# Kernel tuning notes

Hardware: AMD Instinct MI355X
Metric: run time of the kernel (lower is better)

The kernel has to match this reference:

```python
import jax, jax.numpy as jnp
import numpy as np

N, E, IN_C, HID, OUT_C = 50000, 800000, 128, 64, 64
NEG_SLOPE = 0.2
BN_EPS = 1e-5


def _gat(x, edges, W, a_src, a_dst, b):
    """PyG-style GATConv: linear -> per-head attention logits -> softmax over
    incoming edges (self-loops added, as in PyG default) -> weighted scatter-add."""
    n = x.shape[0]
    H, C = a_src.shape
    xw = (x @ W).reshape(n, H, C)                      # [N,H,C]
    loop = jnp.arange(n)
    src = jnp.concatenate([edges[0], loop])            # [E+N]
    dst = jnp.concatenate([edges[1], loop])
    al_s = jnp.sum(xw * a_src, axis=-1)                # [N,H]
    al_d = jnp.sum(xw * a_dst, axis=-1)
    e = jax.nn.leaky_relu(al_s[src] + al_d[dst], NEG_SLOPE)   # [E+N,H]
    emax = jax.ops.segment_max(e, dst, num_segments=n)        # stable softmax per target
    w = jnp.exp(e - emax[dst])
    denom = jax.ops.segment_sum(w, dst, num_segments=n)
    alpha = w / (denom[dst] + 1e-16)                   # [E+N,H]
    msg = xw[src] * alpha[:, :, None]                  # [E+N,H,C]
    out = jax.ops.segment_sum(msg, dst, num_segments=n)       # [N,H,C]
    return out.reshape(n, H * C) + b


def _bn(x, g, be):
    # BatchNorm1d training-mode forward: biased batch statistics over nodes.
    m = jnp.mean(x, axis=0)
    v = jnp.mean((x - m) ** 2, axis=0)
    return (x - m) * jax.lax.rsqrt(v + BN_EPS) * g + be


def setup_inputs() -> dict:
    key = jax.random.key(0)
    ks = jax.random.split(key, 20)
    p = lambda k, s: (jax.random.normal(k, s, jnp.float32) * 0.1)
    return {
        "x": jax.random.normal(ks[0], (1, N, IN_C), jnp.float32),
        "adj": jax.random.randint(ks[1], (2, E), 0, N),
        # conv1: in=128 -> hidden=64, heads=2 (concat -> 128)
        "W1": p(ks[2], (IN_C, 2 * HID)), "as1": p(ks[3], (2, HID)), "ad1": p(ks[4], (2, HID)), "b1": jnp.zeros((2 * HID,), jnp.float32),
        "g1": jnp.ones((2 * HID,), jnp.float32), "be1": jnp.zeros((2 * HID,), jnp.float32),
        # conv2: 128 -> 64, heads=2
        "W2": p(ks[5], (2 * HID, 2 * HID)), "as2": p(ks[6], (2, HID)), "ad2": p(ks[7], (2, HID)), "b2": jnp.zeros((2 * HID,), jnp.float32),
        "g2": jnp.ones((2 * HID,), jnp.float32), "be2": jnp.zeros((2 * HID,), jnp.float32),
        # conv3: 128 -> 64, heads=1
        "W3": p(ks[8], (2 * HID, OUT_C)), "as3": p(ks[9], (1, OUT_C)), "ad3": p(ks[10], (1, OUT_C)), "b3": jnp.zeros((OUT_C,), jnp.float32),
        "g3": jnp.ones((OUT_C,), jnp.float32), "be3": jnp.zeros((OUT_C,), jnp.float32),
    }


def reference(x, adj, W1, as1, ad1, b1, g1, be1, W2, as2, ad2, b2, g2, be2, W3, as3, ad3, b3, g3, be3):
    x0 = x[0]                                          # squeeze batch dim
    x1 = _bn(jax.nn.relu(_gat(x0, adj, W1, as1, ad1, b1)), g1, be1)   # [N,128]
    x2 = _bn(jax.nn.relu(_gat(x1, adj, W2, as2, ad2, b2)), g2, be2)   # [N,128]
    x3 = _bn(jax.nn.relu(_gat(x2, adj, W3, as3, ad3, b3)), g3, be3)   # [N,64]
    return jnp.concatenate([x1, x2, x3], axis=-1)      # [N,320]
```

## Files before the change

### kernel.cpp

```cpp
#include <hip/hip_runtime.h>

typedef unsigned int uint;
typedef unsigned short ushort;


static __device__ __forceinline__ ushort bf16_rne(float x) {
    uint u = __float_as_uint(x);
    return (ushort)((u + 0x7fffu + ((u >> 16) & 1u)) >> 16);
}
static __device__ __forceinline__ float bf16_f(ushort h) {
    return __uint_as_float(((uint)h) << 16);
}

__global__ __launch_bounds__(256) void k_bcount(const int* __restrict__ dst, int e,
                                                int* __restrict__ bcntp) {
    __shared__ int h[512];
    int tid = threadIdx.x;
    h[tid] = 0;
    h[tid + 256] = 0;
    __syncthreads();
    int stride = gridDim.x * 256;
    for (int i = blockIdx.x * 256 + tid; i < e; i += stride)
        atomicAdd(&h[dst[i] >> 7], 1);
    __syncthreads();
    if (h[tid]) atomicAdd(&bcntp[tid * 16], h[tid]);
    if (h[tid + 256]) atomicAdd(&bcntp[(tid + 256) * 16], h[tid + 256]);
}

__global__ __launch_bounds__(512) void k_bscan(const int* __restrict__ bcntp,
                                               int* __restrict__ bbase,
                                               int* __restrict__ bcurp, int nb, int n,
                                               int total, int* __restrict__ row_start) {
    __shared__ int s[512];
    int tid = threadIdx.x;
    int v = 0;
    if (tid < nb) v = bcntp[tid * 16] + min(128, n - (tid << 7));
    s[tid] = v;
    __syncthreads();
    for (int off = 1; off < 512; off <<= 1) {
        int t = (tid >= off) ? s[tid - off] : 0;
        __syncthreads();
        s[tid] += t;
        __syncthreads();
    }
    if (tid < nb) {
        int excl = s[tid] - v;
        bbase[tid] = excl;
        bcurp[tid * 16] = excl;
    }
    if (tid == 0) {
        bbase[nb] = total;
        row_start[n] = total;
    }
}

__global__ __launch_bounds__(512) void k_bscatter(const int* __restrict__ src,
                                                  const int* __restrict__ dst, int e, int n,
                                                  int* __restrict__ bcurp,
                                                  int* __restrict__ pk) {
    __shared__ int hcnt[512], bstart[512], bcursor[512], gbase[512];
    __shared__ int stage[8192];
    int tid = threadIdx.x;
    int total = e + n;
    int nchunk = (total + 8191) >> 13;
    for (int c = blockIdx.x; c < nchunk; c += gridDim.x) {
        int base = c << 13;
        int cnt = min(8192, total - base);
        hcnt[tid] = 0;
        __syncthreads();
        for (int j = tid; j < cnt; j += 512) {
            int i = base + j;
            int d = (i < e) ? dst[i] : (i - e);
            atomicAdd(&hcnt[d >> 7], 1);
        }
        __syncthreads();
        int v = hcnt[tid];
        bstart[tid] = v;
        __syncthreads();
        for (int off = 1; off < 512; off <<= 1) {
            int t = (tid >= off) ? bstart[tid - off] : 0;
            __syncthreads();
            bstart[tid] += t;
            __syncthreads();
        }
        int excl = bstart[tid] - v;
        __syncthreads();
        bstart[tid] = excl;
        bcursor[tid] = excl;
        if (v) gbase[tid] = atomicAdd(&bcurp[tid * 16], v);
        __syncthreads();
        for (int j = tid; j < cnt; j += 512) {
            int i = base + j;
            int d, sv;
            if (i < e) { d = dst[i]; sv = src[i]; }
            else       { d = i - e; sv = d; }
            uint b = (uint)(d >> 7);
            int r = atomicAdd(&bcursor[b], 1);
            stage[r] = (int)((b << 23) | ((uint)(d & 127) << 16) | (uint)sv);
        }
        __syncthreads();
        for (int j = tid; j < cnt; j += 512) {
            int p = stage[j];
            int b = (int)(((uint)p) >> 23);
            pk[gbase[b] + (j - bstart[b])] = p;
        }
        __syncthreads();
    }
}

__global__ __launch_bounds__(256) void k_bfill(const int* __restrict__ pk,
                                               const int* __restrict__ bbase, int n,
                                               int* __restrict__ row_start,
                                               int* __restrict__ col) {
    int b = blockIdx.x;
    int s0 = bbase[b], s1 = bbase[b + 1];
    int seg = s1 - s0;
    int node0 = b << 7;
    int nn = min(128, n - node0);
    int tid = threadIdx.x;
    __shared__ int cnt[128], scn[128];
    __shared__ int colst[4608];
    if (tid < 128) cnt[tid] = 0;
    __syncthreads();
    for (int j = tid; j < seg; j += 256)
        atomicAdd(&cnt[(pk[s0 + j] >> 16) & 127], 1);
    __syncthreads();
    int myc = 0;
    if (tid < 128) { myc = cnt[tid]; scn[tid] = myc; }
    __syncthreads();
    for (int off = 1; off < 128; off <<= 1) {
        int t = (tid >= off && tid < 128) ? scn[tid - off] : 0;
        __syncthreads();
        if (tid < 128) scn[tid] += t;
        __syncthreads();
    }
    int excl = 0;
    if (tid < 128) excl = scn[tid] - myc;
    if (tid < nn) row_start[node0 + tid] = s0 + excl;
    __syncthreads();
    if (tid < 128) cnt[tid] = excl;
    __syncthreads();
    bool big = seg > 4608;
    for (int j = tid; j < seg; j += 256) {
        int p = pk[s0 + j];
        int r = atomicAdd(&cnt[(p >> 16) & 127], 1);
        if (big) col[s0 + r] = p & 0xffff;
        else colst[r] = p & 0xffff;
    }
    if (!big) {
        __syncthreads();
        for (int j = tid; j < seg; j += 256) col[s0 + j] = colst[j];
    }
}

typedef __attribute__((ext_vector_type(8))) short short8;
typedef __attribute__((ext_vector_type(4))) float float4v;

template <int F>
__global__ __launch_bounds__(256) void k_wconv3(const float* __restrict__ W,
                                                const float* __restrict__ sc,
                                                const float* __restrict__ sh, int useBN,
                                                ushort* __restrict__ whi,
                                                ushort* __restrict__ wlo,
                                                float* __restrict__ cvec) {
    int n = (blockIdx.x * blockDim.x + threadIdx.x) >> 6;
    int lane = threadIdx.x & 63;
    if (n >= F) return;
    float c = 0.f;
    if (useBN) {
#pragma unroll
        for (int i = 0; i < 2; i++) {
            int k = lane + i * 64;
            c = fmaf(sh[k], W[k * F + n], c);
        }
#pragma unroll
        for (int off = 32; off; off >>= 1) c += __shfl_xor(c, off);
    }
    if (lane == 0) cvec[n] = c;
    if (lane < 16) {
        int ks = lane >> 2, quad = lane & 3;
        int tg = n >> 4, l15 = n & 15;
        long long off8 = ((long long)((tg * 4 + ks) * 64 + quad * 16 + l15)) * 8;
        short8 h8, l8;
#pragma unroll
        for (int j = 0; j < 8; j++) {
            int k = ks * 32 + quad * 8 + j;
            float w = W[k * F + n];
            float wsv = useBN ? w * sc[k] : w;
            ushort h = bf16_rne(wsv);
            h8[j] = (short)h;
            l8[j] = (short)bf16_rne(wsv - bf16_f(h));
        }
        *(short8*)(whi + off8) = h8;
        *(short8*)(wlo + off8) = l8;
    }
}

static __device__ __forceinline__ void cvt8(const float4& f0, const float4& f1,
                                            short8& hi, short8& lo) {
#define CV8(i, val)                                        \
    {                                                      \
        ushort h_ = bf16_rne(val);                         \
        hi[i] = (short)h_;                                 \
        lo[i] = (short)bf16_rne((val)-bf16_f(h_));         \
    }
    CV8(0, f0.x) CV8(1, f0.y) CV8(2, f0.z) CV8(3, f0.w)
    CV8(4, f1.x) CV8(5, f1.y) CV8(6, f1.z) CV8(7, f1.w)
#undef CV8
}

template <int F, int H>
__global__ __launch_bounds__(256) void k_gemm3(const float* __restrict__ A,
                                               const ushort* __restrict__ whi,
                                               const ushort* __restrict__ wlo,
                                               const float* __restrict__ cvec,
                                               const float* __restrict__ asrc,
                                               const float* __restrict__ adst,
                                               ushort* __restrict__ xwb,
                                               float* __restrict__ al_s,
                                               float* __restrict__ al_d, int M) {
    constexpr bool SPLIT = (F == 128);
    constexpr int RPB = SPLIT ? 32 : 64;
    int tid = threadIdx.x;
    int wave = tid >> 6, lane = tid & 63;
    int quad = lane >> 4, l15 = lane & 15;
    int rg = SPLIT ? (wave >> 1) : wave;
    int half = SPLIT ? (wave & 1) : 0;
    int base = blockIdx.x * RPB + rg * 16;
    int coff = half * 64;
    int tgb = SPLIT ? half * 4 : 0;

    float4v acc[4];
#pragma unroll
    for (int t = 0; t < 4; t++) acc[t] = (float4v){0.f, 0.f, 0.f, 0.f};

    int arow = base + l15;
    bool aval = (arow < M);
    const float* Ap = A + (long long)arow * 128;

#pragma unroll
    for (int ks = 0; ks < 4; ks++) {
        float4 f0 = {0.f, 0.f, 0.f, 0.f}, f1 = {0.f, 0.f, 0.f, 0.f};
        if (aval) {
            f0 = *(const float4*)(Ap + ks * 32 + quad * 8);
            f1 = *(const float4*)(Ap + ks * 32 + quad * 8 + 4);
        }
        short8 ah, al;
        cvt8(f0, f1, ah, al);
#pragma unroll
        for (int t = 0; t < 4; t++) {
            long long boff = ((long long)(((tgb + t) * 4 + ks) * 64 + lane)) * 8;
            short8 bh = *(const short8*)(whi + boff);
            short8 bl = *(const short8*)(wlo + boff);
            acc[t] = __builtin_amdgcn_mfma_f32_16x16x32_bf16(ah, bh, acc[t], 0, 0, 0);
            acc[t] = __builtin_amdgcn_mfma_f32_16x16x32_bf16(ah, bl, acc[t], 0, 0, 0);
            acc[t] = __builtin_amdgcn_mfma_f32_16x16x32_bf16(al, bh, acc[t], 0, 0, 0);
        }
    }

    float cv[4], asl[4], adl[4];
#pragma unroll
    for (int t = 0; t < 4; t++) {
        int n = coff + t * 16 + l15;
        cv[t] = cvec[n];
        asl[t] = asrc[n];
        adl[t] = adst[n];
    }
#pragma unroll
    for (int r = 0; r < 4; r++) {
        int grow = base + quad * 4 + r;
        float v0 = acc[0][r] + cv[0];
        float v1 = acc[1][r] + cv[1];
        float v2 = acc[2][r] + cv[2];
        float v3 = acc[3][r] + cv[3];
        if (grow < M) {
            ushort* xp = xwb + (long long)grow * F + coff + l15;
            xp[0] = bf16_rne(v0);
            xp[16] = bf16_rne(v1);
            xp[32] = bf16_rne(v2);
            xp[48] = bf16_rne(v3);
        }
        float ps = 0.f, pd = 0.f;
        ps = fmaf(v0, asl[0], ps); pd = fmaf(v0, adl[0], pd);
        ps = fmaf(v1, asl[1], ps); pd = fmaf(v1, adl[1], pd);
        ps = fmaf(v2, asl[2], ps); pd = fmaf(v2, adl[2], pd);
        ps = fmaf(v3, asl[3], ps); pd = fmaf(v3, adl[3], pd);
#pragma unroll
        for (int off = 1; off < 16; off <<= 1) {
            ps += __shfl_xor(ps, off);
            pd += __shfl_xor(pd, off);
        }
        if (l15 == 0 && grow < M) {
            al_s[grow * H + half] = ps;
            al_d[grow * H + half] = pd;
        }
    }
}

template <int F, int H>
__global__ __launch_bounds__(256) void k_agg(const uint* __restrict__ xwb,
                      const float* __restrict__ al_s,
                      const float* __restrict__ al_d, const int* __restrict__ row_start,
                      const int* __restrict__ col, const float* __restrict__ bias,
                      float* __restrict__ y, int n) {
    int wid = (blockIdx.x * blockDim.x + threadIdx.x) >> 6;
    int lane = threadIdx.x & 63;
    if (wid >= n) return;
    int beg = row_start[wid], end = row_start[wid + 1];

    float ald[H];
#pragma unroll
    for (int h = 0; h < H; h++) ald[h] = al_d[wid * H + h];

    if (end - beg <= 64) {
        int nb = end - beg;
        int s_c = 0;
        float ev0 = -1e30f, ev1 = -1e30f;
        if (lane < nb) {
            s_c = col[beg + lane];
            if (H == 2) {
                float2 av = ((const float2*)al_s)[s_c];
                float e0 = av.x + ald[0];
                float e1 = av.y + ald[1];
                ev0 = (e0 >= 0.f) ? e0 : 0.2f * e0;
                ev1 = (e1 >= 0.f) ? e1 : 0.2f * e1;
            } else {
                float e0 = al_s[s_c] + ald[0];
                ev0 = (e0 >= 0.f) ? e0 : 0.2f * e0;
            }
        }
        float m0 = ev0, m1 = ev1;
#pragma unroll
        for (int off = 32; off; off >>= 1) {
            m0 = fmaxf(m0, __shfl_xor(m0, off));
            if (H == 2) m1 = fmaxf(m1, __shfl_xor(m1, off));
        }
        float x0 = (lane < nb) ? __expf(ev0 - m0) : 0.f;
        float x1 = (H == 2 && lane < nb) ? __expf(ev1 - m1) : 0.f;
        float l0 = x0, l1 = x1;
#pragma unroll
        for (int off = 32; off; off >>= 1) {
            l0 += __shfl_xor(l0, off);
            if (H == 2) l1 += __shfl_xor(l1, off);
        }
        float a0 = x0 / (l0 + 1e-16f);
        float a1 = (H == 2) ? x1 / (l1 + 1e-16f) : a0;

        float accv0 = 0.f, accv1 = 0.f, accv2 = 0.f, accv3 = 0.f;
        const uint2* xw2 = (const uint2*)xwb;

        if (F == 128) {
            int li = lane & 31;
            int half = lane >> 5;
            bool head0 = (li < 16);
            for (int j = 0; j < nb; j += 16) {
                int rr[8];
                float alq[8];
#pragma unroll
                for (int q = 0; q < 8; q++) {
                    int e = j + 2 * q + half;
                    rr[q] = __shfl(s_c, e);
                    float aa = __shfl(a0, e);
                    float bb = __shfl(a1, e);
                    alq[q] = (H == 2) ? (head0 ? aa : bb) : aa;
                }
                uint2 uu[8];
#pragma unroll
                for (int q = 0; q < 8; q++)
                    uu[q] = xw2[(rr[q] << 5) + li];
#pragma unroll
                for (int q = 0; q < 8; q++) {
                    accv0 = fmaf(alq[q], __uint_as_float(uu[q].x << 16), accv0);
                    accv1 = fmaf(alq[q], __uint_as_float(uu[q].x & 0xffff0000u), accv1);
                    accv2 = fmaf(alq[q], __uint_as_float(uu[q].y << 16), accv2);
                    accv3 = fmaf(alq[q], __uint_as_float(uu[q].y & 0xffff0000u), accv3);
                }
            }
            accv0 += __shfl_xor(accv0, 32);
            accv1 += __shfl_xor(accv1, 32);
            accv2 += __shfl_xor(accv2, 32);
            accv3 += __shfl_xor(accv3, 32);
            if (li == lane) {
                float4 o;
                o.x = fmaxf(accv0 + bias[4 * li + 0], 0.f);
                o.y = fmaxf(accv1 + bias[4 * li + 1], 0.f);
                o.z = fmaxf(accv2 + bias[4 * li + 2], 0.f);
                o.w = fmaxf(accv3 + bias[4 * li + 3], 0.f);
                ((float4*)y)[(long long)wid * 32 + li] = o;
            }
        } else {
            int li = lane & 15;
            int g = lane >> 4;
            for (int j = 0; j < nb; j += 32) {
                int rr[8];
                float alq[8];
#pragma unroll
                for (int q = 0; q < 8; q++) {
                    int e = j + 4 * q + g;
                    rr[q] = __shfl(s_c, e);
                    alq[q] = __shfl(a0, e);
                }
                uint2 uu[8];
#pragma unroll
                for (int q = 0; q < 8; q++)
                    uu[q] = xw2[(rr[q] << 4) + li];
#pragma unroll
                for (int q = 0; q < 8; q++) {
                    accv0 = fmaf(alq[q], __uint_as_float(uu[q].x << 16), accv0);
                    accv1 = fmaf(alq[q], __uint_as_float(uu[q].x & 0xffff0000u), accv1);
                    accv2 = fmaf(alq[q], __uint_as_float(uu[q].y << 16), accv2);
                    accv3 = fmaf(alq[q], __uint_as_float(uu[q].y & 0xffff0000u), accv3);
                }
            }
            accv0 += __shfl_xor(accv0, 16); accv0 += __shfl_xor(accv0, 32);
            accv1 += __shfl_xor(accv1, 16); accv1 += __shfl_xor(accv1, 32);
            accv2 += __shfl_xor(accv2, 16); accv2 += __shfl_xor(accv2, 32);
            accv3 += __shfl_xor(accv3, 16); accv3 += __shfl_xor(accv3, 32);
            if (lane < 16) {
                float4 o;
                o.x = fmaxf(accv0 + bias[4 * li + 0], 0.f);
                o.y = fmaxf(accv1 + bias[4 * li + 1], 0.f);
                o.z = fmaxf(accv2 + bias[4 * li + 2], 0.f);
                o.w = fmaxf(accv3 + bias[4 * li + 3], 0.f);
                ((float4*)y)[(long long)wid * 16 + li] = o;
            }
        }
        return;
    }

    float acc0 = 0.f, acc1 = 0.f;
    {
        float m[H], l[H];
#pragma unroll
        for (int h = 0; h < H; h++) {
            m[h] = -1e30f;
            l[h] = 0.f;
        }
        for (int e = beg + lane; e < end; e += 64) {
            int s = col[e];
#pragma unroll
            for (int h = 0; h < H; h++) {
                float ev = al_s[s * H + h] + ald[h];
                ev = (ev >= 0.f) ? ev : 0.2f * ev;
                if (ev > m[h]) {
                    l[h] = l[h] * __expf(m[h] - ev) + 1.f;
                    m[h] = ev;
                } else {
                    l[h] += __expf(ev - m[h]);
                }
            }
        }
#pragma unroll
        for (int off = 32; off; off >>= 1) {
#pragma unroll
            for (int h = 0; h < H; h++) {
                float mo = __shfl_xor(m[h], off);
                float lo = __shfl_xor(l[h], off);
                float mn = fmaxf(m[h], mo);
                l[h] = l[h] * __expf(m[h] - mn) + lo * __expf(mo - mn);
                m[h] = mn;
            }
        }
        float inv[H];
#pragma unroll
        for (int h = 0; h < H; h++) inv[h] = 1.f / (l[h] + 1e-16f);

        for (int base = beg; base < end; base += 64) {
            int nb = min(64, end - base);
            int ec = min(base + lane, end - 1);
            int s = col[ec];
            float a0, a1;
            {
                float av[H];
#pragma unroll
                for (int h = 0; h < H; h++) {
                    float ev = al_s[s * H + h] + ald[h];
                    ev = (ev >= 0.f) ? ev : 0.2f * ev;
                    av[h] = __expf(ev - m[h]) * inv[h];
                }
                a0 = av[0];
                a1 = av[H - 1];
            }
            int j = 0;
            for (; j + 4 <= nb; j += 4) {
                int s0 = __shfl(s, j + 0), s1 = __shfl(s, j + 1);
                int s2 = __shfl(s, j + 2), s3 = __shfl(s, j + 3);
                float q00 = __shfl(a0, j + 0), q01 = __shfl(a1, j + 0);
                float q10 = __shfl(a0, j + 1), q11 = __shfl(a1, j + 1);
                float q20 = __shfl(a0, j + 2), q21 = __shfl(a1, j + 2);
                float q30 = __shfl(a0, j + 3), q31 = __shfl(a1, j + 3);
                float p0, p1, p2, p3;
                if (H == 2) {
                    p0 = (lane < 32) ? q00 : q01;
                    p1 = (lane < 32) ? q10 : q11;
                    p2 = (lane < 32) ? q20 : q21;
                    p3 = (lane < 32) ? q30 : q31;
                } else {
                    p0 = q00; p1 = q10; p2 = q20; p3 = q30;
                }
                if (F == 128) {
                    uint u0 = xwb[(s0 << 6) + lane];
                    uint u1 = xwb[(s1 << 6) + lane];
                    uint u2 = xwb[(s2 << 6) + lane];
                    uint u3 = xwb[(s3 << 6) + lane];
                    acc0 = fmaf(p0, __uint_as_float(u0 << 16), acc0);
                    acc1 = fmaf(p0, __uint_as_float(u0 & 0xffff0000u), acc1);
                    acc0 = fmaf(p1, __uint_as_float(u1 << 16), acc0);
                    acc1 = fmaf(p1, __uint_as_float(u1 & 0xffff0000u), acc1);
                    acc0 = fmaf(p2, __uint_as_float(u2 << 16), acc0);
                    acc1 = fmaf(p2, __uint_as_float(u2 & 0xffff0000u), acc1);
                    acc0 = fmaf(p3, __uint_as_float(u3 << 16), acc0);
                    acc1 = fmaf(p3, __uint_as_float(u3 & 0xffff0000u), acc1);
                } else {
                    int idx = lane >> 1;
                    bool hi = (lane & 1) != 0;
                    uint u0 = xwb[(s0 << 5) + idx];
                    uint u1 = xwb[(s1 << 5) + idx];
                    uint u2 = xwb[(s2 << 5) + idx];
                    uint u3 = xwb[(s3 << 5) + idx];
                    acc0 = fmaf(p0, __uint_as_float(hi ? (u0 & 0xffff0000u) : (u0 << 16)), acc0);
                    acc0 = fmaf(p1, __uint_as_float(hi ? (u1 & 0xffff0000u) : (u1 << 16)), acc0);
                    acc0 = fmaf(p2, __uint_as_float(hi ? (u2 & 0xffff0000u) : (u2 << 16)), acc0);
                    acc0 = fmaf(p3, __uint_as_float(hi ? (u3 & 0xffff0000u) : (u3 << 16)), acc0);
                }
            }
            for (; j < nb; ++j) {
                int sj = __shfl(s, j);
                float q0 = __shfl(a0, j);
                float q1 = __shfl(a1, j);
                float alpha;
                if (H == 2) {
                    alpha = (lane < 32) ? q0 : q1;
                } else {
                    alpha = q0;
                }
                if (F == 128) {
                    uint u = xwb[(sj << 6) + lane];
                    acc0 = fmaf(alpha, __uint_as_float(u << 16), acc0);
                    acc1 = fmaf(alpha, __uint_as_float(u & 0xffff0000u), acc1);
                } else {
                    uint u = xwb[(sj << 5) + (lane >> 1)];
                    acc0 = fmaf(alpha, __uint_as_float((lane & 1) ? (u & 0xffff0000u) : (u << 16)), acc0);
                }
            }
        }
    }

    if (F == 128) {
        float2 o;
        o.x = fmaxf(acc0 + bias[2 * lane], 0.f);
        o.y = fmaxf(acc1 + bias[2 * lane + 1], 0.f);
        ((float2*)y)[(long long)wid * 64 + lane] = o;
    } else {
        y[(long long)wid * 64 + lane] = fmaxf(acc0 + bias[lane], 0.f);
    }
}

template <int F>
__global__ void k_bn_stats(const float* __restrict__ y, float* __restrict__ sums, int n) {
    constexpr int C4 = F / 4;
    constexpr int NPB = 256 / C4;
    int c4 = threadIdx.x % C4;
    int sub = threadIdx.x / C4;
    float4 s = {0, 0, 0, 0}, s2 = {0, 0, 0, 0};
    for (int node = blockIdx.x * NPB + sub; node < n; node += gridDim.x * NPB) {
        float4 v = ((const float4*)y)[node * C4 + c4];
        s.x += v.x; s.y += v.y; s.z += v.z; s.w += v.w;
        s2.x += v.x * v.x; s2.y += v.y * v.y; s2.z += v.z * v.z; s2.w += v.w * v.w;
    }
    __shared__ float4 ls[256], ls2[256];
    ls[threadIdx.x] = s;
    ls2[threadIdx.x] = s2;
    __syncthreads();
    if (sub == 0) {
#pragma unroll
        for (int k = 1; k < NPB; k++) {
            float4 t = ls[c4 + k * C4], t2 = ls2[c4 + k * C4];
            s.x += t.x; s.y += t.y; s.z += t.z; s.w += t.w;
            s2.x += t2.x; s2.y += t2.y; s2.z += t2.z; s2.w += t2.w;
        }
        atomicAdd(&sums[c4 * 4 + 0], s.x);
        atomicAdd(&sums[c4 * 4 + 1], s.y);
        atomicAdd(&sums[c4 * 4 + 2], s.z);
        atomicAdd(&sums[c4 * 4 + 3], s.w);
        atomicAdd(&sums[F + c4 * 4 + 0], s2.x);
        atomicAdd(&sums[F + c4 * 4 + 1], s2.y);
        atomicAdd(&sums[F + c4 * 4 + 2], s2.z);
        atomicAdd(&sums[F + c4 * 4 + 3], s2.w);
    }
}

template <int F>
__global__ void k_bn_prep(const float* __restrict__ sums, const float* __restrict__ g,
                          const float* __restrict__ be, float* __restrict__ sc,
                          float* __restrict__ sh, float invN) {
    int ch = threadIdx.x;
    if (ch < F) {
        float mean = sums[ch] * invN;
        float var = sums[F + ch] * invN - mean * mean;
        float s = g[ch] * rsqrtf(var + 1e-5f);
        sc[ch] = s;
        sh[ch] = be[ch] - mean * s;
    }
}

template <int F>
__global__ void k_bn_apply(const float* __restrict__ y, const float* __restrict__ sc,
                           const float* __restrict__ sh, float* __restrict__ outp, int n) {
    constexpr int C4 = F / 4;
    int t = blockIdx.x * blockDim.x + threadIdx.x;
    if (t >= n * C4) return;
    int node = t / C4, c4 = t % C4;
    float4 v = ((const float4*)y)[t];
    float4 o;
    o.x = v.x * sc[c4 * 4 + 0] + sh[c4 * 4 + 0];
    o.y = v.y * sc[c4 * 4 + 1] + sh[c4 * 4 + 1];
    o.z = v.z * sc[c4 * 4 + 2] + sh[c4 * 4 + 2];
    o.w = v.w * sc[c4 * 4 + 3] + sh[c4 * 4 + 3];
    ((float4*)(outp + (long long)node * 320))[c4] = o;
}

extern "C" void kernel_launch(void* const* d_in, const int* in_sizes, int n_in,
                              void* d_out, int out_size, void* d_ws, size_t ws_size,
                              hipStream_t stream) {
    const float* x   = (const float*)d_in[0];
    const int*   adj = (const int*)d_in[1];
    const float* W1  = (const float*)d_in[2];
    const float* as1 = (const float*)d_in[3];
    const float* ad1 = (const float*)d_in[4];
    const float* b1  = (const float*)d_in[5];
    const float* g1  = (const float*)d_in[6];
    const float* be1 = (const float*)d_in[7];
    const float* W2  = (const float*)d_in[8];
    const float* as2 = (const float*)d_in[9];
    const float* ad2 = (const float*)d_in[10];
    const float* b2  = (const float*)d_in[11];
    const float* g2  = (const float*)d_in[12];
    const float* be2 = (const float*)d_in[13];
    const float* W3  = (const float*)d_in[14];
    const float* as3 = (const float*)d_in[15];
    const float* ad3 = (const float*)d_in[16];
    const float* b3  = (const float*)d_in[17];
    const float* g3  = (const float*)d_in[18];
    const float* be3 = (const float*)d_in[19];
    float* out = (float*)d_out;

    const int N = in_sizes[0] / 128;
    const int E = in_sizes[1] / 2;

    float* ws    = (float*)d_ws;
    float* ybuf  = ws;
    float* al_s  = ybuf + (size_t)N * 128;
    float* al_d  = al_s + (size_t)N * 2;
    float* stats1 = al_d + (size_t)N * 2;
    float* stats2 = stats1 + 256;
    float* stats3 = stats2 + 256;
    float* scb   = stats3 + 256;
    float* shb   = scb + 128;
    uint* xwb    = (uint*)(shb + 128);
    int* ibase     = (int*)(xwb + (size_t)N * 64);
    int* bcntp     = ibase;
    int* bcurp     = bcntp + 8192;
    int* bbase     = bcurp + 8192;
    int* row_start = ibase + N;
    int* btot      = row_start + (N + 1);
    int* col       = btot + 64;

    uintptr_t wp = (uintptr_t)(col + (E + N));
    wp = (wp + 63) & ~(uintptr_t)63;
    ushort* w1hi = (ushort*)wp;
    ushort* w1lo = w1hi + 16384;
    ushort* w2hi = w1lo + 16384;
    ushort* w2lo = w2hi + 16384;
    ushort* w3hi = w2lo + 16384;
    ushort* w3lo = w3hi + 8192;
    float* c1 = (float*)(w3lo + 8192);
    float* c2 = c1 + 128;
    float* c3 = c2 + 128;

    int* pk = (int*)ybuf;

    const int* esrc = adj;
    const int* edst = adj + E;

    const int B = 256;
    auto cdiv = [](int a, int b) { return (a + b - 1) / b; };

    hipMemsetAsync(stats1, 0, 768 * sizeof(float), stream);

    k_wconv3<128><<<32, 256, 0, stream>>>(W1, nullptr, nullptr, 0, w1hi, w1lo, c1);

    const int NB = (N + 127) >> 7;
    hipMemsetAsync(bcntp, 0, 8192 * sizeof(int), stream);
    k_bcount<<<128, 256, 0, stream>>>(edst, E, bcntp);
    k_bscan<<<1, 512, 0, stream>>>(bcntp, bbase, bcurp, NB, N, E + N, row_start);
    int nchunk = (E + N + 8191) >> 13;
    k_bscatter<<<nchunk, 512, 0, stream>>>(esrc, edst, E, N, bcurp, pk);
    k_bfill<<<NB, 256, 0, stream>>>(pk, bbase, N, row_start, col);

    const float invN = 1.f / (float)N;
    ushort* xwb_us = (ushort*)xwb;

    k_gemm3<128, 2><<<cdiv(N, 32), B, 0, stream>>>(x, w1hi, w1lo, c1,
                                                   as1, ad1, xwb_us, al_s, al_d, N);
    k_agg<128, 2><<<cdiv(N, 4), B, 0, stream>>>(xwb, al_s, al_d, row_start, col, b1, ybuf, N);
    k_bn_stats<128><<<256, B, 0, stream>>>(ybuf, stats1, N);
    k_bn_prep<128><<<1, 128, 0, stream>>>(stats1, g1, be1, scb, shb, invN);
    k_wconv3<128><<<32, 256, 0, stream>>>(W2, scb, shb, 1, w2hi, w2lo, c2);
    k_bn_apply<128><<<cdiv(N * 32, B), B, 0, stream>>>(ybuf, scb, shb, out + 0, N);

    k_gemm3<128, 2><<<cdiv(N, 32), B, 0, stream>>>(ybuf, w2hi, w2lo, c2,
                                                   as2, ad2, xwb_us, al_s, al_d, N);
    k_agg<128, 2><<<cdiv(N, 4), B, 0, stream>>>(xwb, al_s, al_d, row_start, col, b2, ybuf, N);
    k_bn_stats<128><<<256, B, 0, stream>>>(ybuf, stats2, N);
    k_bn_prep<128><<<1, 128, 0, stream>>>(stats2, g2, be2, scb, shb, invN);
    k_wconv3<64><<<16, 256, 0, stream>>>(W3, scb, shb, 1, w3hi, w3lo, c3);
    k_bn_apply<128><<<cdiv(N * 32, B), B, 0, stream>>>(ybuf, scb, shb, out + 128, N);

    k_gemm3<64, 1><<<cdiv(N, 64), B, 0, stream>>>(ybuf, w3hi, w3lo, c3,
                                                  as3, ad3, xwb_us, al_s, al_d, N);
    k_agg<64, 1><<<cdiv(N, 4), B, 0, stream>>>(xwb, al_s, al_d, row_start, col, b3, ybuf, N);
    k_bn_stats<64><<<256, B, 0, stream>>>(ybuf, stats3, N);
    k_bn_prep<64><<<1, 64, 0, stream>>>(stats3, g3, be3, scb, shb, invN);
    k_bn_apply<64><<<cdiv(N * 16, B), B, 0, stream>>>(ybuf, scb, shb, out + 256, N);
}
```

Before: 435.7 us.

## Fuse BatchNorm statistics accumulation into aggregation kernel epilogue

Removes the separate k_bn_stats pass by having each aggregation block accumulate per-channel sum and sum-of-squares in shared memory, then atomically add them into one of 32 global slots. k_bn_prep now reduces across the slots. This avoids re-reading the full N×F activation buffer three times. In exchange it adds shared-memory atomics in the aggregation epilogue, global atomics from every block, and a larger stats buffer to zero.

```diff
diff --git a/kernel.cpp b/kernel.cpp
--- a/kernel.cpp
+++ b/kernel.cpp
@@ -3,6 +3,8 @@
 typedef unsigned int uint;
 typedef unsigned short ushort;
 
+
+#define NSLOT 32
 
 static __device__ __forceinline__ ushort bf16_rne(float x) {
     uint u = __float_as_uint(x);
@@ -302,305 +304,315 @@
                       const float* __restrict__ al_s,
                       const float* __restrict__ al_d, const int* __restrict__ row_start,
                       const int* __restrict__ col, const float* __restrict__ bias,
-                      float* __restrict__ y, int n) {
-    int wid = (blockIdx.x * blockDim.x + threadIdx.x) >> 6;
-    int lane = threadIdx.x & 63;
-    if (wid >= n) return;
-    int beg = row_start[wid], end = row_start[wid + 1];
-
-    float ald[H];
-#pragma unroll
-    for (int h = 0; h < H; h++) ald[h] = al_d[wid * H + h];
-
-    if (end - beg <= 64) {
-        int nb = end - beg;
-        int s_c = 0;
-        float ev0 = -1e30f, ev1 = -1e30f;
-        if (lane < nb) {
-            s_c = col[beg + lane];
-            if (H == 2) {
-                float2 av = ((const float2*)al_s)[s_c];
-                float e0 = av.x + ald[0];
-                float e1 = av.y + ald[1];
-                ev0 = (e0 >= 0.f) ? e0 : 0.2f * e0;
-                ev1 = (e1 >= 0.f) ? e1 : 0.2f * e1;
+                      float* __restrict__ y, float* __restrict__ stats, int n) {
+    __shared__ float lsum[F], lsum2[F];
+    int tid = threadIdx.x;
+    if (tid < F) {
+        lsum[tid] = 0.f;
+        lsum2[tid] = 0.f;
+    }
+    __syncthreads();
+
+    int wid = (blockIdx.x * blockDim.x + tid) >> 6;
+    int lane = tid & 63;
+
+    if (wid < n) {
+        int beg = row_start[wid], end = row_start[wid + 1];
+
+        float ald[H];
+#pragma unroll
+        for (int h = 0; h < H; h++) ald[h] = al_d[wid * H + h];
+
+        if (end - beg <= 64) {
+            int nb = end - beg;
+            int s_c = 0;
+            float ev0 = -1e30f, ev1 = -1e30f;
+            if (lane < nb) {
+                s_c = col[beg + lane];
+                if (H == 2) {
+                    float2 av = ((const float2*)al_s)[s_c];
+                    float e0 = av.x + ald[0];
+                    float e1 = av.y + ald[1];
+                    ev0 = (e0 >= 0.f) ? e0 : 0.2f * e0;
+                    ev1 = (e1 >= 0.f) ? e1 : 0.2f * e1;
+                } else {
+                    float e0 = al_s[s_c] + ald[0];
+                    ev0 = (e0 >= 0.f) ? e0 : 0.2f * e0;
+                }
+            }
+            float m0 = ev0, m1 = ev1;
+#pragma unroll
+            for (int off = 32; off; off >>= 1) {
+                m0 = fmaxf(m0, __shfl_xor(m0, off));
+                if (H == 2) m1 = fmaxf(m1, __shfl_xor(m1, off));
+            }
+            float x0 = (lane < nb) ? __expf(ev0 - m0) : 0.f;
+            float x1 = (H == 2 && lane < nb) ? __expf(ev1 - m1) : 0.f;
+            float l0 = x0, l1 = x1;
+#pragma unroll
+            for (int off = 32; off; off >>= 1) {
+                l0 += __shfl_xor(l0, off);
+                if (H == 2) l1 += __shfl_xor(l1, off);
+            }
+            float a0 = x0 / (l0 + 1e-16f);
+            float a1 = (H == 2) ? x1 / (l1 + 1e-16f) : a0;
+
+            float accv0 = 0.f, accv1 = 0.f, accv2 = 0.f, accv3 = 0.f;
+            const uint2* xw2 = (const uint2*)xwb;
+
+            if (F == 128) {
+                int li = lane & 31;
+                int half = lane >> 5;
+                bool head0 = (li < 16);
+                for (int j = 0; j < nb; j += 16) {
+                    int rr[8];
+                    float alq[8];
+#pragma unroll
+                    for (int q = 0; q < 8; q++) {
+                        int e = j + 2 * q + half;
+                        rr[q] = __shfl(s_c, e);
+                        float aa = __shfl(a0, e);
+                        float bb = __shfl(a1, e);
+                        alq[q] = (H == 2) ? (head0 ? aa : bb) : aa;
+                    }
+                    uint2 uu[8];
+#pragma unroll
+                    for (int q = 0; q < 8; q++)
+                        uu[q] = xw2[(rr[q] << 5) + li];
+#pragma unroll
+                    for (int q = 0; q < 8; q++) {
+                        accv0 = fmaf(alq[q], __uint_as_float(uu[q].x << 16), accv0);
+                        accv1 = fmaf(alq[q], __uint_as_float(uu[q].x & 0xffff0000u), accv1);
+                        accv2 = fmaf(alq[q], __uint_as_float(uu[q].y << 16), accv2);
+                        accv3 = fmaf(alq[q], __uint_as_float(uu[q].y & 0xffff0000u), accv3);
+                    }
+                }
+                accv0 += __shfl_xor(accv0, 32);
+                accv1 += __shfl_xor(accv1, 32);
+                accv2 += __shfl_xor(accv2, 32);
+                accv3 += __shfl_xor(accv3, 32);
+                if (li == lane) {
+                    float4 o;
+                    o.x = fmaxf(accv0 + bias[4 * li + 0], 0.f);
+                    o.y = fmaxf(accv1 + bias[4 * li + 1], 0.f);
+                    o.z = fmaxf(accv2 + bias[4 * li + 2], 0.f);
+                    o.w = fmaxf(accv3 + bias[4 * li + 3], 0.f);
+                    ((float4*)y)[(long long)wid * 32 + li] = o;
+                    atomicAdd(&lsum[4 * li + 0], o.x);
+                    atomicAdd(&lsum[4 * li + 1], o.y);
+                    atomicAdd(&lsum[4 * li + 2], o.z);
+                    atomicAdd(&lsum[4 * li + 3], o.w);
+                    atomicAdd(&lsum2[4 * li + 0], o.x * o.x);
+                    atomicAdd(&lsum2[4 * li + 1], o.y * o.y);
+                    atomicAdd(&lsum2[4 * li + 2], o.z * o.z);
+                    atomicAdd(&lsum2[4 * li + 3], o.w * o.w);
+                }
             } else {
-                float e0 = al_s[s_c] + ald[0];
-                ev0 = (e0 >= 0.f) ? e0 : 0.2f * e0;
-            }
-        }
-        float m0 = ev0, m1 = ev1;
-#pragma unroll
-        for (int off = 32; off; off >>= 1) {
-            m0 = fmaxf(m0, __shfl_xor(m0, off));
-            if (H == 2) m1 = fmaxf(m1, __shfl_xor(m1, off));
-        }
-        float x0 = (lane < nb) ? __expf(ev0 - m0) : 0.f;
-        float x1 = (H == 2 && lane < nb) ? __expf(ev1 - m1) : 0.f;
-        float l0 = x0, l1 = x1;
-#pragma unroll
-        for (int off = 32; off; off >>= 1) {
-            l0 += __shfl_xor(l0, off);
-            if (H == 2) l1 += __shfl_xor(l1, off);
-        }
-        float a0 = x0 / (l0 + 1e-16f);
-        float a1 = (H == 2) ? x1 / (l1 + 1e-16f) : a0;
-
-        float accv0 = 0.f, accv1 = 0.f, accv2 = 0.f, accv3 = 0.f;
-        const uint2* xw2 = (const uint2*)xwb;
-
-        if (F == 128) {
-            int li = lane & 31;
-            int half = lane >> 5;
-            bool head0 = (li < 16);
-            for (int j = 0; j < nb; j += 16) {
-                int rr[8];
-                float alq[8];
-#pragma unroll
-                for (int q = 0; q < 8; q++) {
-                    int e = j + 2 * q + half;
-                    rr[q] = __shfl(s_c, e);
-                    float aa = __shfl(a0, e);
-                    float bb = __shfl(a1, e);
-                    alq[q] = (H == 2) ? (head0 ? aa : bb) : aa;
-                }
-                uint2 uu[8];
-#pragma unroll
-                for (int q = 0; q < 8; q++)
-                    uu[q] = xw2[(rr[q] << 5) + li];
-#pragma unroll
-                for (int q = 0; q < 8; q++) {
-                    accv0 = fmaf(alq[q], __uint_as_float(uu[q].x << 16), accv0);
-                    accv1 = fmaf(alq[q], __uint_as_float(uu[q].x & 0xffff0000u), accv1);
-                    accv2 = fmaf(alq[q], __uint_as_float(uu[q].y << 16), accv2);
-                    accv3 = fmaf(alq[q], __uint_as_float(uu[q].y & 0xffff0000u), accv3);
-                }
-            }
-            accv0 += __shfl_xor(accv0, 32);
-            accv1 += __shfl_xor(accv1, 32);
-            accv2 += __shfl_xor(accv2, 32);
-            accv3 += __shfl_xor(accv3, 32);
-            if (li == lane) {
-                float4 o;
-                o.x = fmaxf(accv0 + bias[4 * li + 0], 0.f);
-                o.y = fmaxf(accv1 + bias[4 * li + 1], 0.f);
-                o.z = fmaxf(accv2 + bias[4 * li + 2], 0.f);
-                o.w = fmaxf(accv3 + bias[4 * li + 3], 0.f);
-                ((float4*)y)[(long long)wid * 32 + li] = o;
+                int li = lane & 15;
+                int g = lane >> 4;
+                for (int j = 0; j < nb; j += 32) {
+                    int rr[8];
+                    float alq[8];
+#pragma unroll
+                    for (int q = 0; q < 8; q++) {
+                        int e = j + 4 * q + g;
+                        rr[q] = __shfl(s_c, e);
+                        alq[q] = __shfl(a0, e);
+                    }
+                    uint2 uu[8];
+#pragma unroll
+                    for (int q = 0; q < 8; q++)
+                        uu[q] = xw2[(rr[q] << 4) + li];
+#pragma unroll
+                    for (int q = 0; q < 8; q++) {
+                        accv0 = fmaf(alq[q], __uint_as_float(uu[q].x << 16), accv0);
+                        accv1 = fmaf(alq[q], __uint_as_float(uu[q].x & 0xffff0000u), accv1);
+                        accv2 = fmaf(alq[q], __uint_as_float(uu[q].y << 16), accv2);
+                        accv3 = fmaf(alq[q], __uint_as_float(uu[q].y & 0xffff0000u), accv3);
+                    }
+                }
+                accv0 += __shfl_xor(accv0, 16); accv0 += __shfl_xor(accv0, 32);
+                accv1 += __shfl_xor(accv1, 16); accv1 += __shfl_xor(accv1, 32);
+                accv2 += __shfl_xor(accv2, 16); accv2 += __shfl_xor(accv2, 32);
+                accv3 += __shfl_xor(accv3, 16); accv3 += __shfl_xor(accv3, 32);
+                if (lane < 16) {
+                    float4 o;
+                    o.x = fmaxf(accv0 + bias[4 * li + 0], 0.f);
+                    o.y = fmaxf(accv1 + bias[4 * li + 1], 0.f);
+                    o.z = fmaxf(accv2 + bias[4 * li + 2], 0.f);
+                    o.w = fmaxf(accv3 + bias[4 * li + 3], 0.f);
+                    ((float4*)y)[(long long)wid * 16 + li] = o;
+                    atomicAdd(&lsum[4 * li + 0], o.x);
+                    atomicAdd(&lsum[4 * li + 1], o.y);
+                    atomicAdd(&lsum[4 * li + 2], o.z);
+                    atomicAdd(&lsum[4 * li + 3], o.w);
+                    atomicAdd(&lsum2[4 * li + 0], o.x * o.x);
+                    atomicAdd(&lsum2[4 * li + 1], o.y * o.y);
+                    atomicAdd(&lsum2[4 * li + 2], o.z * o.z);
+                    atomicAdd(&lsum2[4 * li + 3], o.w * o.w);
+                }
             }
         } else {
-            int li = lane & 15;
-            int g = lane >> 4;
-            for (int j = 0; j < nb; j += 32) {
-                int rr[8];
-                float alq[8];
-#pragma unroll
-                for (int q = 0; q < 8; q++) {
-                    int e = j + 4 * q + g;
-                    rr[q] = __shfl(s_c, e);
-                    alq[q] = __shfl(a0, e);
-                }
-                uint2 uu[8];
-#pragma unroll
-                for (int q = 0; q < 8; q++)
-                    uu[q] = xw2[(rr[q] << 4) + li];
-#pragma unroll
-                for (int q = 0; q < 8; q++) {
-                    accv0 = fmaf(alq[q], __uint_as_float(uu[q].x << 16), accv0);
-                    accv1 = fmaf(alq[q], __uint_as_float(uu[q].x & 0xffff0000u), accv1);
-                    accv2 = fmaf(alq[q], __uint_as_float(uu[q].y << 16), accv2);
-                    accv3 = fmaf(alq[q], __uint_as_float(uu[q].y & 0xffff0000u), accv3);
+            float acc0 = 0.f, acc1 = 0.f;
+            {
+                float m[H], l[H];
+#pragma unroll
+                for (int h = 0; h < H; h++) {
+                    m[h] = -1e30f;
+                    l[h] = 0.f;
+                }
+                for (int e = beg + lane; e < end; e += 64) {
+                    int s = col[e];
+#pragma unroll
+                    for (int h = 0; h < H; h++) {
+                        float ev = al_s[s * H + h] + ald[h];
+                        ev = (ev >= 0.f) ? ev : 0.2f * ev;
+                        if (ev > m[h]) {
+                            l[h] = l[h] * __expf(m[h] - ev) + 1.f;
+                            m[h] = ev;
+                        } else {
+                            l[h] += __expf(ev - m[h]);
+                        }
+                    }
+                }
+#pragma unroll
+                for (int off = 32; off; off >>= 1) {
+#pragma unroll
+                    for (int h = 0; h < H; h++) {
+                        float mo = __shfl_xor(m[h], off);
+                        float lo = __shfl_xor(l[h], off);
+                        float mn = fmaxf(m[h], mo);
+                        l[h] = l[h] * __expf(m[h] - mn) + lo * __expf(mo - mn);
+                        m[h] = mn;
+                    }
+                }
+                float inv[H];
+#pragma unroll
+                for (int h = 0; h < H; h++) inv[h] = 1.f / (l[h] + 1e-16f);
+
+                for (int base = beg; base < end; base += 64) {
+                    int nb = min(64, end - base);
+                    int ec = min(base + lane, end - 1);
+                    int s = col[ec];
+                    float a0, a1;
+                    {
+                        float av[H];
+#pragma unroll
+                        for (int h = 0; h < H; h++) {
+                            float ev = al_s[s * H + h] + ald[h];
+                            ev = (ev >= 0.f) ? ev : 0.2f * ev;
+                            av[h] = __expf(ev - m[h]) * inv[h];
+                        }
+                        a0 = av[0];
+                        a1 = av[H - 1];
+                    }
+                    int j = 0;
+                    for (; j + 4 <= nb; j += 4) {
+                        int s0 = __shfl(s, j + 0), s1 = __shfl(s, j + 1);
+                        int s2 = __shfl(s, j + 2), s3 = __shfl(s, j + 3);
+                        float q00 = __shfl(a0, j + 0), q01 = __shfl(a1, j + 0);
+                        float q10 = __shfl(a0, j + 1), q11 = __shfl(a1, j + 1);
+                        float q20 = __shfl(a0, j + 2), q21 = __shfl(a1, j + 2);
+                        float q30 = __shfl(a0, j + 3), q31 = __shfl(a1, j + 3);
+                        float p0, p1, p2, p3;
+                        if (H == 2) {
+                            p0 = (lane < 32) ? q00 : q01;
+                            p1 = (lane < 32) ? q10 : q11;
+                            p2 = (lane < 32) ? q20 : q21;
+                            p3 = (lane < 32) ? q30 : q31;
+                        } else {
+                            p0 = q00; p1 = q10; p2 = q20; p3 = q30;
+                        }
+                        if (F == 128) {
+                            uint u0 = xwb[(s0 << 6) + lane];
+                            uint u1 = xwb[(s1 << 6) + lane];
+                            uint u2 = xwb[(s2 << 6) + lane];
+                            uint u3 = xwb[(s3 << 6) + lane];
+                            acc0 = fmaf(p0, __uint_as_float(u0 << 16), acc0);
+                            acc1 = fmaf(p0, __uint_as_float(u0 & 0xffff0000u), acc1);
+                            acc0 = fmaf(p1, __uint_as_float(u1 << 16), acc0);
+                            acc1 = fmaf(p1, __uint_as_float(u1 & 0xffff0000u), acc1);
+                            acc0 = fmaf(p2, __uint_as_float(u2 << 16), acc0);
+                            acc1 = fmaf(p2, __uint_as_float(u2 & 0xffff0000u), acc1);
+                            acc0 = fmaf(p3, __uint_as_float(u3 << 16), acc0);
+                            acc1 = fmaf(p3, __uint_as_float(u3 & 0xffff0000u), acc1);
+                        } else {
+                            int idx = lane >> 1;
+                            bool hi = (lane & 1) != 0;
+                            uint u0 = xwb[(s0 << 5) + idx];
+                            uint u1 = xwb[(s1 << 5) + idx];
+                            uint u2 = xwb[(s2 << 5) + idx];
+                            uint u3 = xwb[(s3 << 5) + idx];
+                            acc0 = fmaf(p0, __uint_as_float(hi ? (u0 & 0xffff0000u) : (u0 << 16)), acc0);
+                            acc0 = fmaf(p1, __uint_as_float(hi ? (u1 & 0xffff0000u) : (u1 << 16)), acc0);
+                            acc0 = fmaf(p2, __uint_as_float(hi ? (u2 & 0xffff0000u) : (u2 << 16)), acc0);
+                            acc0 = fmaf(p3, __uint_as_float(hi ? (u3 & 0xffff0000u) : (u3 << 16)), acc0);
+                        }
+                    }
+                    for (; j < nb; ++j) {
+                        int sj = __shfl(s, j);
+                        float q0 = __shfl(a0, j);
+                        float q1 = __shfl(a1, j);
+                        float alpha;
+                        if (H == 2) {
+                            alpha = (lane < 32) ? q0 : q1;
+                        } else {
+                            alpha = q0;
+                        }
+                        if (F == 128) {
+                            uint u = xwb[(sj << 6) + lane];
+                            acc0 = fmaf(alpha, __uint_as_float(u << 16), acc0);
+                            acc1 = fmaf(alpha, __uint_as_float(u & 0xffff0000u), acc1);
+                        } else {
+                            uint u = xwb[(sj << 5) + (lane >> 1)];
+                            acc0 = fmaf(alpha, __uint_as_float((lane & 1) ? (u & 0xffff0000u) : (u << 16)), acc0);
+                        }
+                    }
                 }
             }
-            accv0 += __shfl_xor(accv0, 16); accv0 += __shfl_xor(accv0, 32);
-            accv1 += __shfl_xor(accv1, 16); accv1 += __shfl_xor(accv1, 32);
-            accv2 += __shfl_xor(accv2, 16); accv2 += __shfl_xor(accv2, 32);
-            accv3 += __shfl_xor(accv3, 16); accv3 += __shfl_xor(accv3, 32);
-            if (lane < 16) {
-                float4 o;
-                o.x = fmaxf(accv0 + bias[4 * li + 0], 0.f);
-                o.y = fmaxf(accv1 + bias[4 * li + 1], 0.f);
-                o.z = fmaxf(accv2 + bias[4 * li + 2], 0.f);
-                o.w = fmaxf(accv3 + bias[4 * li + 3], 0.f);
-                ((float4*)y)[(long long)wid * 16 + li] = o;
+
+            if (F == 128) {
+                float2 o;
+                o.x = fmaxf(acc0 + bias[2 * lane], 0.f);
+                o.y = fmaxf(acc1 + bias[2 * lane + 1], 0.f);
+                ((float2*)y)[(long long)wid * 64 + lane] = o;
+                atomicAdd(&lsum[2 * lane + 0], o.x);
+                atomicAdd(&lsum[2 * lane + 1], o.y);
+                atomicAdd(&lsum2[2 * lane + 0], o.x * o.x);
+                atomicAdd(&lsum2[2 * lane + 1], o.y * o.y);
+            } else {
+                float o = fmaxf(acc0 + bias[lane], 0.f);
+                y[(long long)wid * 64 + lane] = o;
+                atomicAdd(&lsum[lane], o);
+                atomicAdd(&lsum2[lane], o * o);
             }
         }
-        return;
-    }
-
-    float acc0 = 0.f, acc1 = 0.f;
-    {
-        float m[H], l[H];
-#pragma unroll
-        for (int h = 0; h < H; h++) {
-            m[h] = -1e30f;
-            l[h] = 0.f;
-        }
-        for (int e = beg + lane; e < end; e += 64) {
-            int s = col[e];
-#pragma unroll
-            for (int h = 0; h < H; h++) {
-                float ev = al_s[s * H + h] + ald[h];
-                ev = (ev >= 0.f) ? ev : 0.2f * ev;
-                if (ev > m[h]) {
-                    l[h] = l[h] * __expf(m[h] - ev) + 1.f;
-                    m[h] = ev;
-                } else {
-                    l[h] += __expf(ev - m[h]);
-                }
-            }
-        }
-#pragma unroll
-        for (int off = 32; off; off >>= 1) {
-#pragma unroll
-            for (int h = 0; h < H; h++) {
-                float mo = __shfl_xor(m[h], off);
-                float lo = __shfl_xor(l[h], off);
-                float mn = fmaxf(m[h], mo);
-                l[h] = l[h] * __expf(m[h] - mn) + lo * __expf(mo - mn);
-                m[h] = mn;
-            }
-        }
-        float inv[H];
-#pragma unroll
-        for (int h = 0; h < H; h++) inv[h] = 1.f / (l[h] + 1e-16f);
-
-        for (int base = beg; base < end; base += 64) {
-            int nb = min(64, end - base);
-            int ec = min(base + lane, end - 1);
-            int s = col[ec];
-            float a0, a1;
-            {
-                float av[H];
-#pragma unroll
-                for (int h = 0; h < H; h++) {
-                    float ev = al_s[s * H + h] + ald[h];
-                    ev = (ev >= 0.f) ? ev : 0.2f * ev;
-                    av[h] = __expf(ev - m[h]) * inv[h];
-                }
-                a0 = av[0];
-                a1 = av[H - 1];
-            }
-            int j = 0;
-            for (; j + 4 <= nb; j += 4) {
-                int s0 = __shfl(s, j + 0), s1 = __shfl(s, j + 1);
-                int s2 = __shfl(s, j + 2), s3 = __shfl(s, j + 3);
-                float q00 = __shfl(a0, j + 0), q01 = __shfl(a1, j + 0);
-                float q10 = __shfl(a0, j + 1), q11 = __shfl(a1, j + 1);
-                float q20 = __shfl(a0, j + 2), q21 = __shfl(a1, j + 2);
-                float q30 = __shfl(a0, j + 3), q31 = __shfl(a1, j + 3);
-                float p0, p1, p2, p3;
-                if (H == 2) {
-                    p0 = (lane < 32) ? q00 : q01;
-                    p1 = (lane < 32) ? q10 : q11;
-                    p2 = (lane < 32) ? q20 : q21;
-                    p3 = (lane < 32) ? q30 : q31;
-                } else {
-                    p0 = q00; p1 = q10; p2 = q20; p3 = q30;
-                }
-                if (F == 128) {
-                    uint u0 = xwb[(s0 << 6) + lane];
-                    uint u1 = xwb[(s1 << 6) + lane];
-                    uint u2 = xwb[(s2 << 6) + lane];
-                    uint u3 = xwb[(s3 << 6) + lane];
-                    acc0 = fmaf(p0, __uint_as_float(u0 << 16), acc0);
-                    acc1 = fmaf(p0, __uint_as_float(u0 & 0xffff0000u), acc1);
-                    acc0 = fmaf(p1, __uint_as_float(u1 << 16), acc0);
-                    acc1 = fmaf(p1, __uint_as_float(u1 & 0xffff0000u), acc1);
-                    acc0 = fmaf(p2, __uint_as_float(u2 << 16), acc0);
-                    acc1 = fmaf(p2, __uint_as_float(u2 & 0xffff0000u), acc1);
-                    acc0 = fmaf(p3, __uint_as_float(u3 << 16), acc0);
-                    acc1 = fmaf(p3, __uint_as_float(u3 & 0xffff0000u), acc1);
-                } else {
-                    int idx = lane >> 1;
-                    bool hi = (lane & 1) != 0;
-                    uint u0 = xwb[(s0 << 5) + idx];
-                    uint u1 = xwb[(s1 << 5) + idx];
-                    uint u2 = xwb[(s2 << 5) + idx];
-                    uint u3 = xwb[(s3 << 5) + idx];
-                    acc0 = fmaf(p0, __uint_as_float(hi ? (u0 & 0xffff0000u) : (u0 << 16)), acc0);
-                    acc0 = fmaf(p1, __uint_as_float(hi ? (u1 & 0xffff0000u) : (u1 << 16)), acc0);
-                    acc0 = fmaf(p2, __uint_as_float(hi ? (u2 & 0xffff0000u) : (u2 << 16)), acc0);
-                    acc0 = fmaf(p3, __uint_as_float(hi ? (u3 & 0xffff0000u) : (u3 << 16)), acc0);
-                }
-            }
-            for (; j < nb; ++j) {
-                int sj = __shfl(s, j);
-                float q0 = __shfl(a0, j);
-                float q1 = __shfl(a1, j);
-                float alpha;
-                if (H == 2) {
-                    alpha = (lane < 32) ? q0 : q1;
-                } else {
-                    alpha = q0;
-                }
-                if (F == 128) {
-                    uint u = xwb[(sj << 6) + lane];
-                    acc0 = fmaf(alpha, __uint_as_float(u << 16), acc0);
-                    acc1 = fmaf(alpha, __uint_as_float(u & 0xffff0000u), acc1);
-                } else {
-                    uint u = xwb[(sj << 5) + (lane >> 1)];
-                    acc0 = fmaf(alpha, __uint_as_float((lane & 1) ? (u & 0xffff0000u) : (u << 16)), acc0);
-                }
-            }
-        }
-    }
-
-    if (F == 128) {
-        float2 o;
-        o.x = fmaxf(acc0 + bias[2 * lane], 0.f);
-        o.y = fmaxf(acc1 + bias[2 * lane + 1], 0.f);
-        ((float2*)y)[(long long)wid * 64 + lane] = o;
-    } else {
-        y[(long long)wid * 64 + lane] = fmaxf(acc0 + bias[lane], 0.f);
+    }
+
+    __syncthreads();
+    float* sl = stats + (blockIdx.x & (NSLOT - 1)) * (2 * F);
+    if (tid < F) {
+        atomicAdd(&sl[tid], lsum[tid]);
+        atomicAdd(&sl[F + tid], lsum2[tid]);
     }
 }
 
 template <int F>
-__global__ void k_bn_stats(const float* __restrict__ y, float* __restrict__ sums, int n) {
-    constexpr int C4 = F / 4;
-    constexpr int NPB = 256 / C4;
-    int c4 = threadIdx.x % C4;
-    int sub = threadIdx.x / C4;
-    float4 s = {0, 0, 0, 0}, s2 = {0, 0, 0, 0};
-    for (int node = blockIdx.x * NPB + sub; node < n; node += gridDim.x * NPB) {
-        float4 v = ((const float4*)y)[node * C4 + c4];
-        s.x += v.x; s.y += v.y; s.z += v.z; s.w += v.w;
-        s2.x += v.x * v.x; s2.y += v.y * v.y; s2.z += v.z * v.z; s2.w += v.w * v.w;
-    }
-    __shared__ float4 ls[256], ls2[256];
-    ls[threadIdx.x] = s;
-    ls2[threadIdx.x] = s2;
-    __syncthreads();
-    if (sub == 0) {
-#pragma unroll
-        for (int k = 1; k < NPB; k++) {
-            float4 t = ls[c4 + k * C4], t2 = ls2[c4 + k * C4];
-            s.x += t.x; s.y += t.y; s.z += t.z; s.w += t.w;
-            s2.x += t2.x; s2.y += t2.y; s2.z += t2.z; s2.w += t2.w;
-        }
-        atomicAdd(&sums[c4 * 4 + 0], s.x);
-        atomicAdd(&sums[c4 * 4 + 1], s.y);
-        atomicAdd(&sums[c4 * 4 + 2], s.z);
-        atomicAdd(&sums[c4 * 4 + 3], s.w);
-        atomicAdd(&sums[F + c4 * 4 + 0], s2.x);
-        atomicAdd(&sums[F + c4 * 4 + 1], s2.y);
-        atomicAdd(&sums[F + c4 * 4 + 2], s2.z);
-        atomicAdd(&sums[F + c4 * 4 + 3], s2.w);
-    }
-}
-
-template <int F>
-__global__ void k_bn_prep(const float* __restrict__ sums, const float* __restrict__ g,
+__global__ void k_bn_prep(const float* __restrict__ stats, const float* __restrict__ g,
                           const float* __restrict__ be, float* __restrict__ sc,
                           float* __restrict__ sh, float invN) {
     int ch = threadIdx.x;
     if (ch < F) {
-        float mean = sums[ch] * invN;
-        float var = sums[F + ch] * invN - mean * mean;
-        float s = g[ch] * rsqrtf(var + 1e-5f);
-        sc[ch] = s;
-        sh[ch] = be[ch] - mean * s;
+        float s = 0.f, s2 = 0.f;
+        for (int k = 0; k < NSLOT; k++) {
+            s += stats[k * 2 * F + ch];
+            s2 += stats[k * 2 * F + F + ch];
+        }
+        float mean = s * invN;
+        float var = s2 * invN - mean * mean;
+        float sv = g[ch] * rsqrtf(var + 1e-5f);
+        sc[ch] = sv;
+        sh[ch] = be[ch] - mean * sv;
     }
 }
 
@@ -653,9 +665,9 @@
     float* al_s  = ybuf + (size_t)N * 128;
     float* al_d  = al_s + (size_t)N * 2;
     float* stats1 = al_d + (size_t)N * 2;
-    float* stats2 = stats1 + 256;
-    float* stats3 = stats2 + 256;
-    float* scb   = stats3 + 256;
+    float* stats2 = stats1 + NSLOT * 256;
+    float* stats3 = stats2 + NSLOT * 256;
+    float* scb   = stats3 + NSLOT * 256;
     float* shb   = scb + 128;
     uint* xwb    = (uint*)(shb + 128);
     int* ibase     = (int*)(xwb + (size_t)N * 64);
@@ -686,7 +698,7 @@
     const int B = 256;
     auto cdiv = [](int a, int b) { return (a + b - 1) / b; };
 
-    hipMemsetAsync(stats1, 0, 768 * sizeof(float), stream);
+    hipMemsetAsync(stats1, 0, (size_t)3 * NSLOT * 256 * sizeof(float), stream);
 
     k_wconv3<128><<<32, 256, 0, stream>>>(W1, nullptr, nullptr, 0, w1hi, w1lo, c1);
 
@@ -703,24 +715,24 @@
 
     k_gemm3<128, 2><<<cdiv(N, 32), B, 0, stream>>>(x, w1hi, w1lo, c1,
                                                    as1, ad1, xwb_us, al_s, al_d, N);
-    k_agg<128, 2><<<cdiv(N, 4), B, 0, stream>>>(xwb, al_s, al_d, row_start, col, b1, ybuf, N);
-    k_bn_stats<128><<<256, B, 0, stream>>>(ybuf, stats1, N);
+    k_agg<128, 2><<<cdiv(N, 4), B, 0, stream>>>(xwb, al_s, al_d, row_start, col, b1,
+                                                ybuf, stats1, N);
     k_bn_prep<128><<<1, 128, 0, stream>>>(stats1, g1, be1, scb, shb, invN);
     k_wconv3<128><<<32, 256, 0, stream>>>(W2, scb, shb, 1, w2hi, w2lo, c2);
     k_bn_apply<128><<<cdiv(N * 32, B), B, 0, stream>>>(ybuf, scb, shb, out + 0, N);
 
     k_gemm3<128, 2><<<cdiv(N, 32), B, 0, stream>>>(ybuf, w2hi, w2lo, c2,
                                                    as2, ad2, xwb_us, al_s, al_d, N);
-    k_agg<128, 2><<<cdiv(N, 4), B, 0, stream>>>(xwb, al_s, al_d, row_start, col, b2, ybuf, N);
-    k_bn_stats<128><<<256, B, 0, stream>>>(ybuf, stats2, N);
+    k_agg<128, 2><<<cdiv(N, 4), B, 0, stream>>>(xwb, al_s, al_d, row_start, col, b2,
+                                                ybuf, stats2, N);
     k_bn_prep<128><<<1, 128, 0, stream>>>(stats2, g2, be2, scb, shb, invN);
     k_wconv3<64><<<16, 256, 0, stream>>>(W3, scb, shb, 1, w3hi, w3lo, c3);
     k_bn_apply<128><<<cdiv(N * 32, B), B, 0, stream>>>(ybuf, scb, shb, out + 128, N);
 
     k_gemm3<64, 1><<<cdiv(N, 64), B, 0, stream>>>(ybuf, w3hi, w3lo, c3,
                                                   as3, ad3, xwb_us, al_s, al_d, N);
-    k_agg<64, 1><<<cdiv(N, 4), B, 0, stream>>>(xwb, al_s, al_d, row_start, col, b3, ybuf, N);
-    k_bn_stats<64><<<256, B, 0, stream>>>(ybuf, stats3, N);
+    k_agg<64, 1><<<cdiv(N, 4), B, 0, stream>>>(xwb, al_s, al_d, row_start, col, b3,
+                                               ybuf, stats3, N);
     k_bn_prep<64><<<1, 64, 0, stream>>>(stats3, g3, be3, scb, shb, invN);
     k_bn_apply<64><<<cdiv(N * 16, B), B, 0, stream>>>(ybuf, scb, shb, out + 256, N);
 }
```

New measurement: 503.6 us. 15.6% more time.
